# Kernel tuning notes

Hardware: AMD Instinct MI355X
Metric: run time of the kernel (lower is better)

Reference implementation:

```python
import jax, jax.numpy as jnp
import numpy as np

NPHEN = 64    # number of expert submodels
K = 32        # len(subset1): selected experts / output columns
B = 2048      # batch size
D_IN = 1024   # input feature dim
HID = 2048    # hidden dim of each expert MLP


def setup_inputs() -> dict:
    key = jax.random.key(0)
    k_x, k_s, k_w1, k_b1, k_w2, k_b2 = jax.random.split(key, 6)
    x = jax.random.normal(k_x, (B, D_IN), dtype=jnp.float32)
    subset1 = jax.random.randint(k_s, (K,), 0, NPHEN, dtype=jnp.int64)
    # Expert parameter banks (one 2-layer MLP per phenotype), scaled like torch defaults
    W1 = jax.random.normal(k_w1, (NPHEN, D_IN, HID), dtype=jnp.float32) / np.sqrt(D_IN)
    b1 = jax.random.normal(k_b1, (NPHEN, HID), dtype=jnp.float32) * 0.01
    W2 = jax.random.normal(k_w2, (NPHEN, HID, 1), dtype=jnp.float32) / np.sqrt(HID)
    b2 = jax.random.normal(k_b2, (NPHEN, 1), dtype=jnp.float32) * 0.01
    return {"x": x, "subset1": subset1, "W1": W1, "b1": b1, "W2": W2, "b2": b2}


def reference(x, subset1, W1, b1, W2, b2):
    # Gather the selected experts' weights: [K, D_IN, HID], [K, HID], [K, HID], [K]
    W1s = W1[subset1]
    b1s = b1[subset1]
    W2s = W2[subset1, :, 0]
    b2s = b2[subset1, 0]
    # Batched grouped matmul replacing the per-column Python loop:
    # h[b,k,h] = relu(sum_d x[b,d] * W1s[k,d,h] + b1s[k,h])
    h = jax.nn.relu(jnp.einsum('bd,kdh->bkh', x, W1s) + b1s[None, :, :])
    # predVector[b,k] = sum_h h[b,k,h] * W2s[k,h] + b2s[k]  (== modelList[subset1[k]](x)[:,0])
    pred = jnp.einsum('bkh,kh->bk', h, W2s) + b2s[None, :]
    return pred
```

## Files before the change

kernel.cpp:

```cpp
#include <hip/hip_runtime.h>

#define D_IN 1024
#define HID  2048
#define KSEL 32

typedef __attribute__((ext_vector_type(8))) short short8;
typedef __attribute__((ext_vector_type(4))) float f32x4;

__device__ __forceinline__ short f2bf(float f) {
  union { float f; unsigned u; } c; c.f = f;
  unsigned u = c.u;
  unsigned r = (u + 0x7fffu + ((u >> 16) & 1u)) >> 16;
  return (short)(r & 0xffffu);
}

__device__ __forceinline__ void load_lds16(const void* g, void* l) {
  __builtin_amdgcn_global_load_lds((const __attribute__((address_space(1))) void*)g,
                                   (__attribute__((address_space(3))) void*)l,
                                   16, 0, 0);
}

__global__ __launch_bounds__(256) void conv_x_kernel(const float* __restrict__ x,
                                                     short* __restrict__ Apanel) {
  int tid = blockIdx.x * 256 + threadIdx.x;
  int k8 = tid & 3;
  int m  = (tid >> 2) & 127;
  int ks = (tid >> 9) & 31;
  int mt = tid >> 14;
  const float* src = x + (size_t)(mt * 128 + m) * D_IN + ks * 32 + k8 * 8;
  short8 v;
#pragma unroll
  for (int j = 0; j < 8; ++j) v[j] = f2bf(src[j]);
  *(short8*)(Apanel + (size_t)tid * 8) = v;
}

__global__ __launch_bounds__(256) void conv_w1_kernel(const float* __restrict__ W1,
                                                      const int* __restrict__ subset,
                                                      short* __restrict__ Bpanel) {
  int bid = blockIdx.x;
  int nt = bid & 15;
  int ks = (bid >> 4) & 31;
  int kk = bid >> 9;
  int p  = subset[kk];

  __shared__ __align__(16) float tile[32][128];
  int t = threadIdx.x;
  int wave = t >> 6, lane = t & 63;

  const float* src = W1 + ((size_t)p * D_IN + ks * 32) * HID + nt * 128;
#pragma unroll
  for (int rr = 0; rr < 4; ++rr) {
    int row = rr * 8 + wave * 2;
    const float* g = src + (size_t)(row + (lane >> 5)) * HID + (lane & 31) * 4;
    load_lds16(g, &tile[row][0]);
  }
  __syncthreads();

  int n  = t >> 1;
  int kh = (t & 1) * 16;
  short8 v0, v1;
#pragma unroll
  for (int dd = 0; dd < 8; ++dd) v0[dd] = f2bf(tile[kh + dd][n]);
#pragma unroll
  for (int dd = 0; dd < 8; ++dd) v1[dd] = f2bf(tile[kh + 8 + dd][n]);
  short* dst = Bpanel + (((size_t)(kk * 16 + nt) * 32) + ks) * 4096 + n * 32 + kh;
  *(short8*)dst       = v0;
  *(short8*)(dst + 8) = v1;
}

__global__ __launch_bounds__(256) void init_out_kernel(const int* __restrict__ subset,
                                                       const float* __restrict__ b2,
                                                       float* __restrict__ out) {
  int i = blockIdx.x * 256 + threadIdx.x;
  out[i] = b2[subset[i & 31]];
}

__global__ __launch_bounds__(256) void gemm_kernel(const short* __restrict__ Apanel,
                                                   const short* __restrict__ Bpanel,
                                                   const int* __restrict__ subset,
                                                   const float* __restrict__ b1,
                                                   const float* __restrict__ W2,
                                                   float* __restrict__ out) {
  __shared__ __align__(16) short Atile[4096];
  __shared__ __align__(16) short Btile[4096];

  int id = blockIdx.x;
  int xcd = id & 7;
  int chunk = id >> 3;
  int kk = xcd * 4 + (chunk >> 8);
  int nt = (chunk >> 4) & 15;
  int mt = chunk & 15;

  int tid  = threadIdx.x;
  int wave = tid >> 6;
  int lane = tid & 63;
  int wm = wave >> 1, wn = wave & 1;
  int ml = lane & 15;
  int kq = lane >> 4;

  const short* Abase = Apanel + (size_t)mt * (32 * 4096);
  const short* Bbase = Bpanel + (size_t)((kk * 16 + nt)) * (32 * 4096);

  short* AldsBase0 = Atile + (wave * 64) * 8;
  short* AldsBase1 = Atile + (256 + wave * 64) * 8;
  short* BldsBase0 = Btile + (wave * 64) * 8;
  short* BldsBase1 = Btile + (256 + wave * 64) * 8;

  f32x4 acc[4][4] = {};

  const short8* Ar = (const short8*)Atile;
  const short8* Br = (const short8*)Btile;
  int arow = wm * 64 + ml;
  int brow = wn * 64 + ml;

  for (int ks = 0; ks < 32; ++ks) {
    const short* ga = Abase + ks * 4096;
    const short* gb = Bbase + ks * 4096;
    load_lds16(ga + tid * 8,         AldsBase0);
    load_lds16(ga + (256 + tid) * 8, AldsBase1);
    load_lds16(gb + tid * 8,         BldsBase0);
    load_lds16(gb + (256 + tid) * 8, BldsBase1);
    __syncthreads();

    short8 a[4], b[4];
#pragma unroll
    for (int ti = 0; ti < 4; ++ti) a[ti] = Ar[(arow + ti * 16) * 4 + kq];
#pragma unroll
    for (int tj = 0; tj < 4; ++tj) b[tj] = Br[(brow + tj * 16) * 4 + kq];
#pragma unroll
    for (int ti = 0; ti < 4; ++ti)
#pragma unroll
      for (int tj = 0; tj < 4; ++tj)
        acc[ti][tj] = __builtin_amdgcn_mfma_f32_16x16x32_bf16(a[ti], b[tj],
                                                              acc[ti][tj], 0, 0, 0);
    __syncthreads();
  }

  int sk = subset[kk];
  const float* b1p = b1 + (size_t)sk * HID + nt * 128 + wn * 64;
  const float* w2p = W2 + (size_t)sk * HID + nt * 128 + wn * 64;
  float b1v[4], w2v[4];
#pragma unroll
  for (int tj = 0; tj < 4; ++tj) {
    int n = tj * 16 + ml;
    b1v[tj] = b1p[n];
    w2v[tj] = w2p[n];
  }
  float part[4][4];
#pragma unroll
  for (int ti = 0; ti < 4; ++ti)
#pragma unroll
    for (int r = 0; r < 4; ++r) {
      float s = 0.f;
#pragma unroll
      for (int tj = 0; tj < 4; ++tj) {
        float h = acc[ti][tj][r] + b1v[tj];
        h = h > 0.f ? h : 0.f;
        s += h * w2v[tj];
      }
      part[ti][r] = s;
    }
#pragma unroll
  for (int off = 1; off < 16; off <<= 1) {
#pragma unroll
    for (int ti = 0; ti < 4; ++ti)
#pragma unroll
      for (int r = 0; r < 4; ++r)
        part[ti][r] += __shfl_xor(part[ti][r], off, 64);
  }
  if (ml == 0) {
    int mbase = mt * 128 + wm * 64 + kq * 4;
#pragma unroll
    for (int ti = 0; ti < 4; ++ti)
#pragma unroll
      for (int r = 0; r < 4; ++r)
        atomicAdd(out + (size_t)(mbase + ti * 16 + r) * KSEL + kk, part[ti][r]);
  }
}

extern "C" void kernel_launch(void* const* d_in, const int* in_sizes, int n_in,
                              void* d_out, int out_size, void* d_ws, size_t ws_size,
                              hipStream_t stream) {
  const float* x      = (const float*)d_in[0];
  const int*   subset = (const int*)d_in[1];
  const float* W1     = (const float*)d_in[2];
  const float* b1     = (const float*)d_in[3];
  const float* W2     = (const float*)d_in[4];
  const float* b2     = (const float*)d_in[5];
  float* out = (float*)d_out;

  short* Apanel = (short*)d_ws;
  short* Bpanel = (short*)((char*)d_ws + (size_t)4 * 1024 * 1024);

  conv_x_kernel<<<1024, 256, 0, stream>>>(x, Apanel);
  conv_w1_kernel<<<16384, 256, 0, stream>>>(W1, subset, Bpanel);
  init_out_kernel<<<256, 256, 0, stream>>>(subset, b2, out);
  gemm_kernel<<<8192, 256, 0, stream>>>(Apanel, Bpanel, subset, b1, W2, out);
}
```

Baseline: 1.009 ms.

## Enlarge GEMM tiles to 256x256 with double-buffered LDS and phased prefetch

The GEMM tile grows from 128x128 to 256x256 with 512 threads (8 waves, each covering 128x64), and the A/B panel layouts are rearranged to match. LDS is double-buffered over 64-wide K steps, with global-to-LDS loads issued one stage ahead and interleaved with MFMA phases under explicit waitcnt/barrier scheduling and s_setprio. The aim is to hide global-load latency, raise arithmetic intensity, and cut the number of atomic epilogue writes. The cost is 128KB of LDS per block and higher register pressure from 32 accumulators, which limits occupancy.

```diff
diff --git a/kernel.cpp b/kernel.cpp
--- a/kernel.cpp
+++ b/kernel.cpp
@@ -23,11 +23,12 @@
 __global__ __launch_bounds__(256) void conv_x_kernel(const float* __restrict__ x,
                                                      short* __restrict__ Apanel) {
   int tid = blockIdx.x * 256 + threadIdx.x;
-  int k8 = tid & 3;
-  int m  = (tid >> 2) & 127;
-  int ks = (tid >> 9) & 31;
-  int mt = tid >> 14;
-  const float* src = x + (size_t)(mt * 128 + m) * D_IN + ks * 32 + k8 * 8;
+  int k8  = tid & 3;
+  int m   = (tid >> 2) & 255;
+  int ks2 = (tid >> 10) & 1;
+  int kt  = (tid >> 11) & 15;
+  int mt  = tid >> 15;
+  const float* src = x + (size_t)(mt * 256 + m) * D_IN + kt * 64 + ks2 * 32 + k8 * 8;
   short8 v;
 #pragma unroll
   for (int j = 0; j < 8; ++j) v[j] = f2bf(src[j]);
@@ -38,16 +39,18 @@
                                                       const int* __restrict__ subset,
                                                       short* __restrict__ Bpanel) {
   int bid = blockIdx.x;
-  int nt = bid & 15;
-  int ks = (bid >> 4) & 31;
+  int hg = bid & 15;
+  int dg = (bid >> 4) & 31;
   int kk = bid >> 9;
   int p  = subset[kk];
+  int nt = hg >> 1;
+  int nh = hg & 1;
 
   __shared__ __align__(16) float tile[32][128];
   int t = threadIdx.x;
   int wave = t >> 6, lane = t & 63;
 
-  const float* src = W1 + ((size_t)p * D_IN + ks * 32) * HID + nt * 128;
+  const float* src = W1 + ((size_t)p * D_IN + dg * 32) * HID + hg * 128;
 #pragma unroll
   for (int rr = 0; rr < 4; ++rr) {
     int row = rr * 8 + wave * 2;
@@ -63,7 +66,8 @@
   for (int dd = 0; dd < 8; ++dd) v0[dd] = f2bf(tile[kh + dd][n]);
 #pragma unroll
   for (int dd = 0; dd < 8; ++dd) v1[dd] = f2bf(tile[kh + 8 + dd][n]);
-  short* dst = Bpanel + (((size_t)(kk * 16 + nt) * 32) + ks) * 4096 + n * 32 + kh;
+  short* dst = Bpanel + (((size_t)(kk * 8 + nt) * 32) + dg) * 8192
+             + (nh * 128 + n) * 32 + kh;
   *(short8*)dst       = v0;
   *(short8*)(dst + 8) = v1;
 }
@@ -75,107 +79,141 @@
   out[i] = b2[subset[i & 31]];
 }
 
-__global__ __launch_bounds__(256) void gemm_kernel(const short* __restrict__ Apanel,
-                                                   const short* __restrict__ Bpanel,
-                                                   const int* __restrict__ subset,
-                                                   const float* __restrict__ b1,
-                                                   const float* __restrict__ W2,
-                                                   float* __restrict__ out) {
-  __shared__ __align__(16) short Atile[4096];
-  __shared__ __align__(16) short Btile[4096];
+__global__ __launch_bounds__(512, 2) void gemm_kernel(const short* __restrict__ Apanel,
+                                                      const short* __restrict__ Bpanel,
+                                                      const int* __restrict__ subset,
+                                                      const float* __restrict__ b1,
+                                                      const float* __restrict__ W2,
+                                                      float* __restrict__ out) {
+  __shared__ __align__(16) short lds[2][4][8192];
 
   int id = blockIdx.x;
   int xcd = id & 7;
   int chunk = id >> 3;
-  int kk = xcd * 4 + (chunk >> 8);
-  int nt = (chunk >> 4) & 15;
-  int mt = chunk & 15;
+  int kk = xcd * 4 + (chunk >> 6);
+  int rem = chunk & 63;
+  int nt = rem >> 3;
+  int mt = rem & 7;
 
   int tid  = threadIdx.x;
   int wave = tid >> 6;
   int lane = tid & 63;
-  int wm = wave >> 1, wn = wave & 1;
+  int wm = wave >> 2, wn = wave & 3;
   int ml = lane & 15;
   int kq = lane >> 4;
 
-  const short* Abase = Apanel + (size_t)mt * (32 * 4096);
-  const short* Bbase = Bpanel + (size_t)((kk * 16 + nt)) * (32 * 4096);
-
-  short* AldsBase0 = Atile + (wave * 64) * 8;
-  short* AldsBase1 = Atile + (256 + wave * 64) * 8;
-  short* BldsBase0 = Btile + (wave * 64) * 8;
-  short* BldsBase1 = Btile + (256 + wave * 64) * 8;
-
-  f32x4 acc[4][4] = {};
-
-  const short8* Ar = (const short8*)Atile;
-  const short8* Br = (const short8*)Btile;
-  int arow = wm * 64 + ml;
-  int brow = wn * 64 + ml;
-
-  for (int ks = 0; ks < 32; ++ks) {
-    const short* ga = Abase + ks * 4096;
-    const short* gb = Bbase + ks * 4096;
-    load_lds16(ga + tid * 8,         AldsBase0);
-    load_lds16(ga + (256 + tid) * 8, AldsBase1);
-    load_lds16(gb + tid * 8,         BldsBase0);
-    load_lds16(gb + (256 + tid) * 8, BldsBase1);
-    __syncthreads();
-
-    short8 a[4], b[4];
-#pragma unroll
-    for (int ti = 0; ti < 4; ++ti) a[ti] = Ar[(arow + ti * 16) * 4 + kq];
-#pragma unroll
-    for (int tj = 0; tj < 4; ++tj) b[tj] = Br[(brow + tj * 16) * 4 + kq];
-#pragma unroll
-    for (int ti = 0; ti < 4; ++ti)
-#pragma unroll
-      for (int tj = 0; tj < 4; ++tj)
-        acc[ti][tj] = __builtin_amdgcn_mfma_f32_16x16x32_bf16(a[ti], b[tj],
-                                                              acc[ti][tj], 0, 0, 0);
-    __syncthreads();
-  }
+  const short* Abase = Apanel + (size_t)mt * (16 * 2 * 8192);
+  const short* Bbase = Bpanel + (size_t)(kk * 8 + nt) * (16 * 2 * 8192);
+
+#define AU(kt, ks2) (Abase + (((kt) * 2 + (ks2)) << 13))
+#define BU(kt, ks2) (Bbase + (((kt) * 2 + (ks2)) << 13))
+
+#define STAGE_UNIT(SLOT, UNIT, GSRC) do {                                  \
+    const short* _g = (GSRC) + tid * 8;                                    \
+    load_lds16(_g,        &lds[SLOT][UNIT][wave * 512]);                   \
+    load_lds16(_g + 4096, &lds[SLOT][UNIT][wave * 512 + 4096]);            \
+  } while (0)
+
+  f32x4 acc[8][4] = {};
+  short8 a[4], b[4];
+
+  int arow0 = wm * 128 + ml;
+  int brow0 = wn * 64 + ml;
+
+#define PHASE(CS, K2, MH, SS, SU, SG, DOB, DOVM) do {                      \
+    const short* _ua = &lds[CS][K2][0];                                    \
+    _Pragma("unroll")                                                      \
+    for (int q = 0; q < 4; ++q)                                            \
+      a[q] = *(const short8*)(_ua + ((arow0 + (MH * 4 + q) * 16) * 4 + kq) * 8); \
+    if (DOB) {                                                             \
+      const short* _ub = &lds[CS][2 + K2][0];                              \
+      _Pragma("unroll")                                                    \
+      for (int q = 0; q < 4; ++q)                                          \
+        b[q] = *(const short8*)(_ub + ((brow0 + q * 16) * 4 + kq) * 8);    \
+    }                                                                      \
+    STAGE_UNIT(SS, SU, SG);                                                \
+    __builtin_amdgcn_sched_barrier(0);                                     \
+    if (DOVM) asm volatile("s_waitcnt vmcnt(4)" ::: "memory");             \
+    __builtin_amdgcn_s_barrier();                                          \
+    __builtin_amdgcn_sched_barrier(0);                                     \
+    __builtin_amdgcn_s_setprio(1);                                         \
+    _Pragma("unroll")                                                      \
+    for (int i = 0; i < 4; ++i)                                            \
+      _Pragma("unroll")                                                    \
+      for (int j = 0; j < 4; ++j)                                          \
+        acc[MH * 4 + i][j] = __builtin_amdgcn_mfma_f32_16x16x32_bf16(      \
+            a[i], b[j], acc[MH * 4 + i][j], 0, 0, 0);                      \
+    __builtin_amdgcn_s_setprio(0);                                         \
+    __builtin_amdgcn_sched_barrier(0);                                     \
+  } while (0)
+
+  STAGE_UNIT(0, 0, AU(0, 0));
+  STAGE_UNIT(0, 2, BU(0, 0));
+  STAGE_UNIT(0, 1, AU(0, 1));
+  STAGE_UNIT(0, 3, BU(0, 1));
+  __builtin_amdgcn_sched_barrier(0);
+  asm volatile("s_waitcnt vmcnt(4)" ::: "memory");
+  __builtin_amdgcn_s_barrier();
+  __builtin_amdgcn_sched_barrier(0);
+
+  for (int t2 = 0; t2 < 8; ++t2) {
+    int ktA = 2 * t2 + 1;
+    int ktB = (t2 < 7) ? 2 * t2 + 2 : 15;
+    PHASE(0, 0, 0, 1, 0, AU(ktA, 0), 1, 0);
+    PHASE(0, 0, 1, 1, 2, BU(ktA, 0), 0, 1);
+    PHASE(0, 1, 0, 1, 1, AU(ktA, 1), 1, 0);
+    PHASE(0, 1, 1, 1, 3, BU(ktA, 1), 0, 1);
+    PHASE(1, 0, 0, 0, 0, AU(ktB, 0), 1, 0);
+    PHASE(1, 0, 1, 0, 2, BU(ktB, 0), 0, 1);
+    PHASE(1, 1, 0, 0, 1, AU(ktB, 1), 1, 0);
+    PHASE(1, 1, 1, 0, 3, BU(ktB, 1), 0, 1);
+  }
+  asm volatile("s_waitcnt vmcnt(0)" ::: "memory");
 
   int sk = subset[kk];
-  const float* b1p = b1 + (size_t)sk * HID + nt * 128 + wn * 64;
-  const float* w2p = W2 + (size_t)sk * HID + nt * 128 + wn * 64;
+  const float* b1p = b1 + (size_t)sk * HID + nt * 256 + wn * 64;
+  const float* w2p = W2 + (size_t)sk * HID + nt * 256 + wn * 64;
   float b1v[4], w2v[4];
 #pragma unroll
-  for (int tj = 0; tj < 4; ++tj) {
-    int n = tj * 16 + ml;
-    b1v[tj] = b1p[n];
-    w2v[tj] = w2p[n];
-  }
-  float part[4][4];
-#pragma unroll
-  for (int ti = 0; ti < 4; ++ti)
+  for (int nf = 0; nf < 4; ++nf) {
+    int n = nf * 16 + ml;
+    b1v[nf] = b1p[n];
+    w2v[nf] = w2p[n];
+  }
+  float part[8][4];
+#pragma unroll
+  for (int mf = 0; mf < 8; ++mf)
 #pragma unroll
     for (int r = 0; r < 4; ++r) {
       float s = 0.f;
 #pragma unroll
-      for (int tj = 0; tj < 4; ++tj) {
-        float h = acc[ti][tj][r] + b1v[tj];
+      for (int nf = 0; nf < 4; ++nf) {
+        float h = acc[mf][nf][r] + b1v[nf];
         h = h > 0.f ? h : 0.f;
-        s += h * w2v[tj];
+        s += h * w2v[nf];
       }
-      part[ti][r] = s;
+      part[mf][r] = s;
     }
 #pragma unroll
   for (int off = 1; off < 16; off <<= 1) {
 #pragma unroll
-    for (int ti = 0; ti < 4; ++ti)
+    for (int mf = 0; mf < 8; ++mf)
 #pragma unroll
       for (int r = 0; r < 4; ++r)
-        part[ti][r] += __shfl_xor(part[ti][r], off, 64);
+        part[mf][r] += __shfl_xor(part[mf][r], off, 64);
   }
   if (ml == 0) {
-    int mbase = mt * 128 + wm * 64 + kq * 4;
-#pragma unroll
-    for (int ti = 0; ti < 4; ++ti)
+    int mbase = mt * 256 + wm * 128 + kq * 4;
+#pragma unroll
+    for (int mf = 0; mf < 8; ++mf)
 #pragma unroll
       for (int r = 0; r < 4; ++r)
-        atomicAdd(out + (size_t)(mbase + ti * 16 + r) * KSEL + kk, part[ti][r]);
-  }
+        atomicAdd(out + (size_t)(mbase + mf * 16 + r) * KSEL + kk, part[mf][r]);
+  }
+#undef PHASE
+#undef STAGE_UNIT
+#undef AU
+#undef BU
 }
 
 extern "C" void kernel_launch(void* const* d_in, const int* in_sizes, int n_in,
@@ -195,5 +233,5 @@
   conv_x_kernel<<<1024, 256, 0, stream>>>(x, Apanel);
   conv_w1_kernel<<<16384, 256, 0, stream>>>(W1, subset, Bpanel);
   init_out_kernel<<<256, 256, 0, stream>>>(subset, b2, out);
-  gemm_kernel<<<8192, 256, 0, stream>>>(Apanel, Bpanel, subset, b1, W2, out);
-}
+  gemm_kernel<<<2048, 512, 0, stream>>>(Apanel, Bpanel, subset, b1, W2, out);
+}
```

Result: faster. 886.2 us (-12.2%).
